# Performance work log

Hardware: AMD Instinct MI355X
Metric: run time of the kernel (lower is better)

Reference implementation:

```python
import jax, jax.numpy as jnp
import numpy as np

D_MODEL = 2048
N_Q_HEADS = 32
N_KV_HEADS = 8
D_HEAD = 64
D_MLP = 8192
NORM_EPS = 1e-5
INIT_RANGE = 0.02
IGNORE = -100000.0
B, S = 2, 2048


def setup_inputs() -> dict:
    key = jax.random.key(0)
    ks = jax.random.split(key, 8)
    return {
        "resid_pre": jax.random.normal(ks[0], (B, S, D_MODEL), dtype=jnp.float32),
        "W_Q": jax.random.normal(ks[1], (N_Q_HEADS, D_MODEL, D_HEAD), dtype=jnp.float32) * INIT_RANGE,
        "W_K": jax.random.normal(ks[2], (N_KV_HEADS, D_MODEL, D_HEAD), dtype=jnp.float32) * INIT_RANGE,
        "W_V": jax.random.normal(ks[3], (N_KV_HEADS, D_MODEL, D_HEAD), dtype=jnp.float32) * INIT_RANGE,
        "W_O": jax.random.normal(ks[4], (N_KV_HEADS, D_HEAD, D_MODEL), dtype=jnp.float32) * INIT_RANGE,
        "g1": jnp.ones((D_MODEL,), jnp.float32),
        "b1": jnp.zeros((D_MODEL,), jnp.float32),
        "g2": jnp.ones((D_MODEL,), jnp.float32),
        "b2": jnp.zeros((D_MODEL,), jnp.float32),
        "W_in": jax.random.normal(ks[5], (D_MODEL, D_MLP), dtype=jnp.float32) * INIT_RANGE,
        "b_in": jnp.zeros((D_MLP,), jnp.float32),
        "W_out": jax.random.normal(ks[6], (D_MLP, D_MODEL), dtype=jnp.float32) * INIT_RANGE,
        "b_out": jnp.zeros((D_MODEL,), jnp.float32),
    }


def rmsnorm(x, g, b):
    # torch.var (unbiased=False) is mean-centered variance, but x itself is
    # divided (not centered) -- faithful to the source.
    mu = jnp.mean(x, axis=-1, keepdims=True)
    var = jnp.mean(jnp.square(x - mu), axis=-1, keepdims=True)
    std = jnp.sqrt(var + NORM_EPS)
    return (x / std) * g + b


def attention(x, W_Q, W_K, W_V, W_O):
    b, s, _ = x.shape
    q = jnp.einsum('bpd,hde->bphe', x, W_Q)            # [b, s, n_q, d_head]
    k = jnp.einsum('bpd,hde->bphe', x, W_K)            # [b, s, n_kv, d_head]
    v = jnp.einsum('bpd,hde->bphe', x, W_V)            # [b, s, n_kv, d_head]
    g_size = N_Q_HEADS // N_KV_HEADS
    # rearrange '(n_kv g) d' with n_kv outer, group inner
    q = q.reshape(b, s, N_KV_HEADS, g_size, D_HEAD)
    # source einsum sums over the group dim (g not in output) -- faithful
    scores = jnp.einsum('bqkgd,bskd->bkqs', q, k) / jnp.sqrt(jnp.float32(D_HEAD))
    mask = jnp.triu(jnp.ones((s, s), dtype=bool), k=1)
    scores = jnp.where(mask, jnp.float32(IGNORE), scores)
    pattern = jax.nn.softmax(scores, axis=-1)          # [b, n_kv, q, s]
    z = jnp.einsum('bskd,bkqs->bqkd', v, pattern)      # [b, q, n_kv, d_head]
    return jnp.einsum('bqkd,kde->bqe', z, W_O)


def ffn(x, W_in, b_in, W_out, b_out):
    pre = jnp.einsum('bpd,dm->bpm', x, W_in) + b_in
    post = jax.nn.relu(pre)
    return jnp.einsum('bpm,md->bpd', post, W_out) + b_out


def reference(resid_pre, W_Q, W_K, W_V, W_O, g1, b1, g2, b2, W_in, b_in, W_out, b_out):
    resid_mid = attention(rmsnorm(resid_pre, g1, b1), W_Q, W_K, W_V, W_O) + resid_pre
    resid_post = ffn(rmsnorm(resid_mid, g2, b2), W_in, b_in, W_out, b_out) + resid_mid
    return resid_post
```

## Files before the change

### kernel.cpp

```cpp
#include <hip/hip_runtime.h>
#include <hip/hip_bf16.h>


using bf16 = __hip_bfloat16;
typedef __bf16 bf16x8_t __attribute__((ext_vector_type(8)));
typedef float  f32x4_t  __attribute__((ext_vector_type(4)));

#define D_MODEL 2048
#define SEQ     2048
#define NB      2
#define NTOK    4096
#define NKV     8
#define DHEAD   64
#define DMLP    8192
#define NQKV    1536

__device__ inline void storev(float* p, float v) { *p = v; }
__device__ inline void storev(bf16* p, float v)  { *p = __float2bfloat16(v); }

__device__ inline bf16 h_from_b(__bf16 x) {
    union { __bf16 b; bf16 h; } u;
    u.b = x;
    return u.h;
}

__global__ __launch_bounds__(256) void transpose_f32_bf16_kernel(
    const float* __restrict__ in, bf16* __restrict__ out, int K, int N)
{
    __shared__ float tile[32][33];
    const int n0 = blockIdx.x * 32, k0 = blockIdx.y * 32;
    const int tx = threadIdx.x & 31, ty = threadIdx.x >> 5;
    #pragma unroll
    for (int i = 0; i < 32; i += 8)
        tile[ty + i][tx] = in[(size_t)(k0 + ty + i) * N + n0 + tx];
    __syncthreads();
    #pragma unroll
    for (int i = 0; i < 32; i += 8)
        out[(size_t)(n0 + ty + i) * K + k0 + tx] = __float2bfloat16(tile[tx][ty + i]);
}

__global__ __launch_bounds__(256) void rmsnorm_kernel(
    const float* __restrict__ x, const float* __restrict__ g,
    const float* __restrict__ b, bf16* __restrict__ out)
{
    const int row = blockIdx.x;
    const int t = threadIdx.x;
    const float* xr = x + (size_t)row * D_MODEL;
    float4 a0 = *reinterpret_cast<const float4*>(xr + t * 8);
    float4 a1 = *reinterpret_cast<const float4*>(xr + t * 8 + 4);
    float v[8] = {a0.x, a0.y, a0.z, a0.w, a1.x, a1.y, a1.z, a1.w};
    float sum = 0.f, sumsq = 0.f;
    #pragma unroll
    for (int j = 0; j < 8; ++j) { sum += v[j]; sumsq += v[j] * v[j]; }
    #pragma unroll
    for (int o = 1; o < 64; o <<= 1) {
        sum   += __shfl_xor(sum, o);
        sumsq += __shfl_xor(sumsq, o);
    }
    __shared__ float rs[4], rq[4];
    if ((t & 63) == 0) { rs[t >> 6] = sum; rq[t >> 6] = sumsq; }
    __syncthreads();
    sum   = rs[0] + rs[1] + rs[2] + rs[3];
    sumsq = rq[0] + rq[1] + rq[2] + rq[3];
    const float mu  = sum * (1.f / D_MODEL);
    const float var = sumsq * (1.f / D_MODEL) - mu * mu;
    const float rstd = 1.f / sqrtf(var + 1e-5f);
    const int c = t * 8;
    float4 g0 = *reinterpret_cast<const float4*>(g + c);
    float4 g1 = *reinterpret_cast<const float4*>(g + c + 4);
    float4 b0 = *reinterpret_cast<const float4*>(b + c);
    float4 b1 = *reinterpret_cast<const float4*>(b + c + 4);
    float gg[8] = {g0.x, g0.y, g0.z, g0.w, g1.x, g1.y, g1.z, g1.w};
    float bb[8] = {b0.x, b0.y, b0.z, b0.w, b1.x, b1.y, b1.z, b1.w};
    bf16* op = out + (size_t)row * D_MODEL + c;
    #pragma unroll
    for (int j = 0; j < 8; ++j) op[j] = __float2bfloat16(v[j] * rstd * gg[j] + bb[j]);
}

__global__ __launch_bounds__(256) void fusedA_kernel(
    const float* __restrict__ resid_pre, const float* __restrict__ g1,
    const float* __restrict__ b1, bf16* __restrict__ x1,
    const float* __restrict__ WQ, const float* __restrict__ WK,
    const float* __restrict__ WV, bf16* __restrict__ wqkvT,
    const float* __restrict__ WO, bf16* __restrict__ woT)
{
    __shared__ __align__(16) float smem[32 * 65];
    const int id = blockIdx.x;
    const int t  = threadIdx.x;

    if (id < 4096) {
        float* rs = smem;
        float* rq = smem + 4;
        const float* xr = resid_pre + (size_t)id * D_MODEL;
        float4 a0 = *reinterpret_cast<const float4*>(xr + t * 8);
        float4 a1 = *reinterpret_cast<const float4*>(xr + t * 8 + 4);
        float v[8] = {a0.x, a0.y, a0.z, a0.w, a1.x, a1.y, a1.z, a1.w};
        float sum = 0.f, sumsq = 0.f;
        #pragma unroll
        for (int j = 0; j < 8; ++j) { sum += v[j]; sumsq += v[j] * v[j]; }
        #pragma unroll
        for (int o = 1; o < 64; o <<= 1) {
            sum   += __shfl_xor(sum, o);
            sumsq += __shfl_xor(sumsq, o);
        }
        if ((t & 63) == 0) { rs[t >> 6] = sum; rq[t >> 6] = sumsq; }
        __syncthreads();
        sum   = rs[0] + rs[1] + rs[2] + rs[3];
        sumsq = rq[0] + rq[1] + rq[2] + rq[3];
        const float mu  = sum * (1.f / D_MODEL);
        const float var = sumsq * (1.f / D_MODEL) - mu * mu;
        const float rstd = 1.f / sqrtf(var + 1e-5f);
        const int c = t * 8;
        float4 g0 = *reinterpret_cast<const float4*>(g1 + c);
        float4 g1v = *reinterpret_cast<const float4*>(g1 + c + 4);
        float4 b0 = *reinterpret_cast<const float4*>(b1 + c);
        float4 b1v = *reinterpret_cast<const float4*>(b1 + c + 4);
        float gg[8] = {g0.x, g0.y, g0.z, g0.w, g1v.x, g1v.y, g1v.z, g1v.w};
        float bb[8] = {b0.x, b0.y, b0.z, b0.w, b1v.x, b1v.y, b1v.z, b1v.w};
        bf16* op = x1 + (size_t)id * D_MODEL + c;
        #pragma unroll
        for (int j = 0; j < 8; ++j) op[j] = __float2bfloat16(v[j] * rstd * gg[j] + bb[j]);
    } else if (id < 5632) {
        int sub = id - 4096;
        const int which = sub >> 9;
        sub &= 511;
        const float* in = which == 0 ? WQ : (which == 1 ? WK : WV);
        bf16* outp = wqkvT + (size_t)which * 512 * D_MODEL;
        const int ngroup = which == 0 ? 4 : 1;
        const int kv = sub >> 6;
        const int k0 = (sub & 63) * 32;
        float (*tile)[65] = reinterpret_cast<float(*)[65]>(smem);
        const int e  = t & 63, kk = t >> 6;
        #pragma unroll
        for (int i = 0; i < 32; i += 4) {
            float s = 0.f;
            for (int g = 0; g < ngroup; ++g)
                s += in[((size_t)(kv * ngroup + g) * 2048 + k0 + kk + i) * 64 + e];
            tile[kk + i][e] = s;
        }
        __syncthreads();
        const int k = t & 31, ee = t >> 5;
        #pragma unroll
        for (int i = 0; i < 64; i += 8)
            outp[(size_t)(kv * 64 + ee + i) * 2048 + k0 + k] = __float2bfloat16(tile[k][ee + i]);
    } else {
        const int sub = id - 5632;
        const int n0 = (sub & 63) * 32, k0 = (sub >> 6) * 32;
        float (*tile)[33] = reinterpret_cast<float(*)[33]>(smem);
        const int tx = t & 31, ty = t >> 5;
        #pragma unroll
        for (int i = 0; i < 32; i += 8)
            tile[ty + i][tx] = WO[(size_t)(k0 + ty + i) * D_MODEL + n0 + tx];
        __syncthreads();
        #pragma unroll
        for (int i = 0; i < 32; i += 8)
            woT[(size_t)(n0 + ty + i) * 512 + k0 + tx] = __float2bfloat16(tile[tx][ty + i]);
    }
}

template<int BM, int BN, typename TC, bool BIAS, bool RELU, bool RESID>
__global__ __launch_bounds__(512, 2) void gemm_pipe_kernel(
    const bf16* __restrict__ A, const bf16* __restrict__ Bt,
    TC* __restrict__ C, const float* __restrict__ bias,
    const float* __restrict__ resid, int M, int N, int K, int nbx)
{
    constexpr int BK   = 64;
    constexpr int MREP = BM / 32;
    constexpr int NREP = BN / 64;
    constexpr int AI   = (BM * BK) / 4096;
    constexpr int BI   = (BN * BK) / 4096;
    constexpr int LD   = AI + BI;

    __shared__ __align__(16) bf16 As[2][BM * BK];
    __shared__ __align__(16) bf16 Bs[2][BN * BK];

    const int nwg = gridDim.x;
    const int swz = (blockIdx.x & 7) * (nwg >> 3) + (blockIdx.x >> 3);
    const int nby = nwg / nbx;
    const int by  = swz % nby;
    const int bx  = swz / nby;
    const int row0 = by * BM, col0 = bx * BN;

    const int t  = threadIdx.x;
    const int w  = t >> 6, ln = t & 63;
    const int wm = w >> 2, wn = w & 3;
    const int lr = ln & 15, hi = ln >> 4;

    const int srow = w * 8 + (ln >> 3);
    const int skx  = ((ln & 7) ^ (ln >> 3)) * 8;

    f32x4_t acc[MREP][NREP];
    #pragma unroll
    for (int m = 0; m < MREP; ++m)
        #pragma unroll
        for (int n = 0; n < NREP; ++n) acc[m][n] = (f32x4_t){0.f, 0.f, 0.f, 0.f};

    const int NT = K / BK;

    {
        const bf16* ga = A  + (size_t)(row0 + srow) * K + skx;
        const bf16* gb = Bt + (size_t)(col0 + srow) * K + skx;
        #pragma unroll
        for (int i = 0; i < AI; ++i)
            __builtin_amdgcn_global_load_lds(
                (const __attribute__((address_space(1))) void*)(ga + (size_t)i * 64 * K),
                (__attribute__((address_space(3))) void*)(&As[0][i * 4096 + w * 512]), 16, 0, 0);
        #pragma unroll
        for (int i = 0; i < BI; ++i)
            __builtin_amdgcn_global_load_lds(
                (const __attribute__((address_space(1))) void*)(gb + (size_t)i * 64 * K),
                (__attribute__((address_space(3))) void*)(&Bs[0][i * 4096 + w * 512]), 16, 0, 0);
    }

    for (int tt = 0; tt < NT; ++tt) {
        const int c = tt & 1;
        asm volatile("s_waitcnt lgkmcnt(0)" ::: "memory");
        __builtin_amdgcn_sched_barrier(0);
        __builtin_amdgcn_s_barrier();
        __builtin_amdgcn_sched_barrier(0);
        if (tt + 1 < NT) {
            const int d = c ^ 1;
            const int kt = (tt + 1) * BK;
            const bf16* ga = A  + (size_t)(row0 + srow) * K + kt + skx;
            const bf16* gb = Bt + (size_t)(col0 + srow) * K + kt + skx;
            #pragma unroll
            for (int i = 0; i < AI; ++i)
                __builtin_amdgcn_global_load_lds(
                    (const __attribute__((address_space(1))) void*)(ga + (size_t)i * 64 * K),
                    (__attribute__((address_space(3))) void*)(&As[d][i * 4096 + w * 512]), 16, 0, 0);
            #pragma unroll
            for (int i = 0; i < BI; ++i)
                __builtin_amdgcn_global_load_lds(
                    (const __attribute__((address_space(1))) void*)(gb + (size_t)i * 64 * K),
                    (__attribute__((address_space(3))) void*)(&Bs[d][i * 4096 + w * 512]), 16, 0, 0);
            __builtin_amdgcn_sched_barrier(0);
            if constexpr (LD == 8)      asm volatile("s_waitcnt vmcnt(8)" ::: "memory");
            else if constexpr (LD == 6) asm volatile("s_waitcnt vmcnt(6)" ::: "memory");
            else if constexpr (LD == 4) asm volatile("s_waitcnt vmcnt(4)" ::: "memory");
            else                        asm volatile("s_waitcnt vmcnt(3)" ::: "memory");
        } else {
            asm volatile("s_waitcnt vmcnt(0)" ::: "memory");
        }
        __builtin_amdgcn_sched_barrier(0);
        __builtin_amdgcn_s_barrier();
        __builtin_amdgcn_sched_barrier(0);

        #pragma unroll
        for (int kk = 0; kk < 2; ++kk) {
            bf16x8_t af[MREP], bfr[NREP];
            #pragma unroll
            for (int m = 0; m < MREP; ++m) {
                const int row = wm * (BM / 2) + m * 16 + lr;
                af[m] = *reinterpret_cast<const bf16x8_t*>(
                    &As[c][row * 64 + ((kk * 32 + hi * 8) ^ ((row & 7) << 3))]);
            }
            #pragma unroll
            for (int n = 0; n < NREP; ++n) {
                const int col = wn * (BN / 4) + n * 16 + lr;
                bfr[n] = *reinterpret_cast<const bf16x8_t*>(
                    &Bs[c][col * 64 + ((kk * 32 + hi * 8) ^ ((col & 7) << 3))]);
            }
            #pragma unroll
            for (int m = 0; m < MREP; ++m)
                #pragma unroll
                for (int n = 0; n < NREP; ++n)
                    acc[m][n] = __builtin_amdgcn_mfma_f32_16x16x32_bf16(af[m], bfr[n], acc[m][n], 0, 0, 0);
        }
    }

    #pragma unroll
    for (int m = 0; m < MREP; ++m) {
        #pragma unroll
        for (int n = 0; n < NREP; ++n) {
            const int cgl = col0 + wn * (BN / 4) + n * 16 + lr;
            #pragma unroll
            for (int j = 0; j < 4; ++j) {
                const int r = row0 + wm * (BM / 2) + m * 16 + hi * 4 + j;
                float v = acc[m][n][j];
                if constexpr (BIAS)  v += bias[cgl];
                if constexpr (RELU)  v = fmaxf(v, 0.f);
                if constexpr (RESID) v += resid[(size_t)r * N + cgl];
                storev(&C[(size_t)r * N + cgl], v);
            }
        }
    }
}

template<typename TC, bool BIAS, bool RELU, bool RESID>
__global__ __launch_bounds__(512, 2) void gemm_8ph_kernel(
    const bf16* __restrict__ A, const bf16* __restrict__ Bt,
    TC* __restrict__ C, const float* __restrict__ bias,
    const float* __restrict__ resid, int M, int N, int K, int nbx)
{
    __shared__ __align__(16) bf16 As[2][256 * 64];
    __shared__ __align__(16) bf16 Bs[2][256 * 64];

    const int nwg = gridDim.x;
    const int swz = (blockIdx.x & 7) * (nwg >> 3) + (blockIdx.x >> 3);
    const int nby = nwg / nbx;
    const int by  = swz % nby;
    const int bx  = swz / nby;
    const int row0 = by * 256, col0 = bx * 256;

    const int t  = threadIdx.x;
    const int w  = t >> 6, ln = t & 63;
    const int wm = w >> 2, wn = w & 3;
    const int lr = ln & 15, hi = ln >> 4;
    const int rx = (lr & 7) << 3;

    const int srow = w * 8 + (ln >> 3);
    const int skx  = ((ln & 7) ^ (ln >> 3)) * 8;

#define STAGE_A8(u, dbuf, kt)                                                   \
    __builtin_amdgcn_global_load_lds(                                           \
        (const __attribute__((address_space(1))) void*)(A + (size_t)(row0 + (u) * 64 + srow) * K + (kt) + skx), \
        (__attribute__((address_space(3))) void*)(&As[dbuf][(u) * 4096 + w * 512]), 16, 0, 0)
#define STAGE_B8(u, dbuf, kt)                                                   \
    __builtin_amdgcn_global_load_lds(                                           \
        (const __attribute__((address_space(1))) void*)(Bt + (size_t)(col0 + (u) * 64 + srow) * K + (kt) + skx), \
        (__attribute__((address_space(3))) void*)(&Bs[dbuf][(u) * 4096 + w * 512]), 16, 0, 0)
#define PH_BAR                                                                  \
    __builtin_amdgcn_sched_barrier(0);                                          \
    __builtin_amdgcn_s_barrier();                                               \
    __builtin_amdgcn_sched_barrier(0)
#define LGKM0                                                                   \
    asm volatile("s_waitcnt lgkmcnt(0)" ::: "memory");                          \
    __builtin_amdgcn_sched_barrier(0)

    f32x4_t acc[8][4];
    #pragma unroll
    for (int m = 0; m < 8; ++m)
        #pragma unroll
        for (int n = 0; n < 4; ++n) acc[m][n] = (f32x4_t){0.f, 0.f, 0.f, 0.f};

    bf16x8_t af[4][2];
    bf16x8_t af2[4][2];
    bf16x8_t bfr[4][2];

    const int NT = K / 64;

    STAGE_A8(0, 0, 0); STAGE_A8(2, 0, 0);
    STAGE_B8(0, 0, 0); STAGE_B8(1, 0, 0); STAGE_B8(2, 0, 0); STAGE_B8(3, 0, 0);
    STAGE_A8(1, 0, 0); STAGE_A8(3, 0, 0);
    asm volatile("s_waitcnt vmcnt(2)" ::: "memory");
    PH_BAR;

    for (int tt = 0; tt < NT; ++tt) {
        const int c  = tt & 1, d = c ^ 1;
        const int kn = (tt + 1) * 64;
        const bool pf = (tt + 1 < NT);

        #pragma unroll
        for (int mq = 0; mq < 4; ++mq) {
            const int row = wm * 128 + mq * 16 + lr;
            #pragma unroll
            for (int kk = 0; kk < 2; ++kk)
                af[mq][kk] = *reinterpret_cast<const bf16x8_t*>(
                    &As[c][row * 64 + ((kk * 32 + hi * 8) ^ rx)]);
        }
        #pragma unroll
        for (int n = 0; n < 2; ++n) {
            const int col = wn * 64 + n * 16 + lr;
            #pragma unroll
            for (int kk = 0; kk < 2; ++kk)
                bfr[n][kk] = *reinterpret_cast<const bf16x8_t*>(
                    &Bs[c][col * 64 + ((kk * 32 + hi * 8) ^ rx)]);
        }
        if (pf) { STAGE_A8(0, d, kn); STAGE_A8(2, d, kn); }
        PH_BAR;
        LGKM0;
        __builtin_amdgcn_s_setprio(1);
        #pragma unroll
        for (int mq = 0; mq < 4; ++mq)
            #pragma unroll
            for (int n = 0; n < 2; ++n)
                #pragma unroll
                for (int kk = 0; kk < 2; ++kk)
                    acc[mq][n] = __builtin_amdgcn_mfma_f32_16x16x32_bf16(af[mq][kk], bfr[n][kk], acc[mq][n], 0, 0, 0);
        __builtin_amdgcn_s_setprio(0);

        #pragma unroll
        for (int n = 2; n < 4; ++n) {
            const int col = wn * 64 + n * 16 + lr;
            #pragma unroll
            for (int kk = 0; kk < 2; ++kk)
                bfr[n][kk] = *reinterpret_cast<const bf16x8_t*>(
                    &Bs[c][col * 64 + ((kk * 32 + hi * 8) ^ rx)]);
        }
        if (pf) { STAGE_B8(0, d, kn); STAGE_B8(1, d, kn); }
        __builtin_amdgcn_sched_barrier(0);
        if (pf) { asm volatile("s_waitcnt vmcnt(4)" ::: "memory"); }
        else    { asm volatile("s_waitcnt vmcnt(0)" ::: "memory"); }
        PH_BAR;
        LGKM0;
        __builtin_amdgcn_s_setprio(1);
        #pragma unroll
        for (int mq = 0; mq < 4; ++mq)
            #pragma unroll
            for (int n = 2; n < 4; ++n)
                #pragma unroll
                for (int kk = 0; kk < 2; ++kk)
                    acc[mq][n] = __builtin_amdgcn_mfma_f32_16x16x32_bf16(af[mq][kk], bfr[n][kk], acc[mq][n], 0, 0, 0);
        __builtin_amdgcn_s_setprio(0);

        #pragma unroll
        for (int mq = 0; mq < 4; ++mq) {
            const int row = wm * 128 + 64 + mq * 16 + lr;
            #pragma unroll
            for (int kk = 0; kk < 2; ++kk)
                af2[mq][kk] = *reinterpret_cast<const bf16x8_t*>(
                    &As[c][row * 64 + ((kk * 32 + hi * 8) ^ rx)]);
        }
        if (pf) { STAGE_B8(2, d, kn); STAGE_B8(3, d, kn); }
        PH_BAR;
        LGKM0;
        __builtin_amdgcn_s_setprio(1);
        #pragma unroll
        for (int mq = 0; mq < 4; ++mq)
            #pragma unroll
            for (int n = 2; n < 4; ++n)
                #pragma unroll
                for (int kk = 0; kk < 2; ++kk)
                    acc[4 + mq][n] = __builtin_amdgcn_mfma_f32_16x16x32_bf16(af2[mq][kk], bfr[n][kk], acc[4 + mq][n], 0, 0, 0);
        __builtin_amdgcn_s_setprio(0);

        if (pf) {
            STAGE_A8(1, d, kn); STAGE_A8(3, d, kn);
            __builtin_amdgcn_sched_barrier(0);
            asm volatile("s_waitcnt vmcnt(2)" ::: "memory");
        }
        PH_BAR;
        __builtin_amdgcn_s_setprio(1);
        #pragma unroll
        for (int mq = 0; mq < 4; ++mq)
            #pragma unroll
            for (int n = 0; n < 2; ++n)
                #pragma unroll
                for (int kk = 0; kk < 2; ++kk)
                    acc[4 + mq][n] = __builtin_amdgcn_mfma_f32_16x16x32_bf16(af2[mq][kk], bfr[n][kk], acc[4 + mq][n], 0, 0, 0);
        __builtin_amdgcn_s_setprio(0);
    }

    #pragma unroll
    for (int m = 0; m < 8; ++m) {
        #pragma unroll
        for (int n = 0; n < 4; ++n) {
            const int cgl = col0 + wn * 64 + n * 16 + lr;
            #pragma unroll
            for (int j = 0; j < 4; ++j) {
                const int r = row0 + wm * 128 + m * 16 + hi * 4 + j;
                float v = acc[m][n][j];
                if constexpr (BIAS)  v += bias[cgl];
                if constexpr (RELU)  v = fmaxf(v, 0.f);
                if constexpr (RESID) v += resid[(size_t)r * N + cgl];
                storev(&C[(size_t)r * N + cgl], v);
            }
        }
    }
#undef STAGE_A8
#undef STAGE_B8
#undef PH_BAR
#undef LGKM0
}

#define KVBLK 64
#define LP    72

__global__ __launch_bounds__(256) void fusedB_kernel(
    const bf16* __restrict__ qkv, bf16* __restrict__ z,
    const float* __restrict__ W_in, bf16* __restrict__ winT)
{
    __shared__ __align__(16) char smem[3 * KVBLK * LP * 2];

    if (blockIdx.x >= 256) {
        const int sub = blockIdx.x - 256;
        const int n0 = (sub & 255) * 32, k0 = (sub >> 8) * 32;
        float (*tile)[33] = reinterpret_cast<float(*)[33]>(smem);
        const int tx = threadIdx.x & 31, ty = threadIdx.x >> 5;
        #pragma unroll
        for (int i = 0; i < 32; i += 8)
            tile[ty + i][tx] = W_in[(size_t)(k0 + ty + i) * DMLP + n0 + tx];
        __syncthreads();
        #pragma unroll
        for (int i = 0; i < 32; i += 8)
            winT[(size_t)(n0 + ty + i) * D_MODEL + k0 + tx] = __float2bfloat16(tile[tx][ty + i]);
        return;
    }

    const int i_   = blockIdx.x;
    const int pair = (i_ & 7) | ((i_ >> 7) << 3);
    const int a    = (i_ >> 3) & 15;
    const int kv   = pair & 7;
    const int b    = pair >> 3;
    const int b2   = 31 - a;
    const int t  = threadIdx.x;
    const int w  = t >> 6;
    const int ln = t & 63;
    const int lr = ln & 15;
    const int hi = ln >> 4;
    const int lk = hi * 8;

    bf16* Ks = reinterpret_cast<bf16*>(smem);
    bf16* Vt = Ks + KVBLK * LP;
    bf16* Ps = Vt + DHEAD * LP;

    bf16x8_t qfA[2], qfB[2];
    #pragma unroll
    for (int sb = 0; sb < 2; ++sb) {
        const int qrow = (sb ? b2 : a) * 64 + w * 16 + lr;
        const bf16* qp = qkv + (size_t)(b * SEQ + qrow) * NQKV + kv * 64;
        #pragma unroll
        for (int kk = 0; kk < 2; ++kk) {
            bf16x8_t v = *reinterpret_cast<const bf16x8_t*>(qp + kk * 32 + lk);
            if (sb) qfB[kk] = v; else qfA[kk] = v;
        }
    }

    f32x4_t accA[4], accB[4];
    #pragma unroll
    for (int n = 0; n < 4; ++n) {
        accA[n] = (f32x4_t){0.f, 0.f, 0.f, 0.f};
        accB[n] = (f32x4_t){0.f, 0.f, 0.f, 0.f};
    }
    float mA[4] = {-1e30f, -1e30f, -1e30f, -1e30f}, lA[4] = {0.f, 0.f, 0.f, 0.f};
    float mB[4] = {-1e30f, -1e30f, -1e30f, -1e30f}, lB[4] = {0.f, 0.f, 0.f, 0.f};

    const int qcdA = a  * 64 + w * 16 + hi * 4;
    const int qcdB = b2 * 64 + w * 16 + hi * 4;

    auto process = [&](const bf16x8_t* qf, f32x4_t* acc_o, float* m_st,
                       float* l_st, int qcd, int k0g, bool diag) {
        f32x4_t s[4];
        #pragma unroll
        for (int n = 0; n < 4; ++n) s[n] = (f32x4_t){0.f, 0.f, 0.f, 0.f};
        #pragma unroll
        for (int kk = 0; kk < 2; ++kk) {
            #pragma unroll
            for (int n = 0; n < 4; ++n) {
                bf16x8_t kf = *reinterpret_cast<const bf16x8_t*>(&Ks[(n * 16 + lr) * LP + kk * 32 + lk]);
                s[n] = __builtin_amdgcn_mfma_f32_16x16x32_bf16(qf[kk], kf, s[n], 0, 0, 0);
            }
        }
        #pragma unroll
        for (int n = 0; n < 4; ++n) {
            const int colg = k0g + n * 16 + lr;
            #pragma unroll
            for (int j = 0; j < 4; ++j) {
                float val = s[n][j] * 0.125f;
                if (diag && colg > qcd + j) val = -1e30f;
                s[n][j] = val;
            }
        }
        float alpha[4], mnew[4];
        #pragma unroll
        for (int j = 0; j < 4; ++j) {
            float mx = fmaxf(fmaxf(s[0][j], s[1][j]), fmaxf(s[2][j], s[3][j]));
            mx = fmaxf(mx, __shfl_xor(mx, 1));
            mx = fmaxf(mx, __shfl_xor(mx, 2));
            mx = fmaxf(mx, __shfl_xor(mx, 4));
            mx = fmaxf(mx, __shfl_xor(mx, 8));
            mnew[j]  = fmaxf(m_st[j], mx);
            alpha[j] = __expf(m_st[j] - mnew[j]);
            m_st[j]  = mnew[j];
        }
        float psum[4] = {0.f, 0.f, 0.f, 0.f};
        #pragma unroll
        for (int n = 0; n < 4; ++n) {
            #pragma unroll
            for (int j = 0; j < 4; ++j) {
                float p = __expf(s[n][j] - mnew[j]);
                psum[j] += p;
                Ps[(w * 16 + hi * 4 + j) * LP + n * 16 + lr] = __float2bfloat16(p);
            }
        }
        #pragma unroll
        for (int j = 0; j < 4; ++j) {
            float ps = psum[j];
            ps += __shfl_xor(ps, 1);
            ps += __shfl_xor(ps, 2);
            ps += __shfl_xor(ps, 4);
            ps += __shfl_xor(ps, 8);
            l_st[j] = l_st[j] * alpha[j] + ps;
        }
        #pragma unroll
        for (int n = 0; n < 4; ++n)
            #pragma unroll
            for (int j = 0; j < 4; ++j)
                acc_o[n][j] *= alpha[j];
        #pragma unroll
        for (int kk = 0; kk < 2; ++kk) {
            bf16x8_t pa = *reinterpret_cast<const bf16x8_t*>(&Ps[(w * 16 + lr) * LP + kk * 32 + lk]);
            #pragma unroll
            for (int n = 0; n < 4; ++n) {
                bf16x8_t vf = *reinterpret_cast<const bf16x8_t*>(&Vt[(n * 16 + lr) * LP + kk * 32 + lk]);
                acc_o[n] = __builtin_amdgcn_mfma_f32_16x16x32_bf16(pa, vf, acc_o[n], 0, 0, 0);
            }
        }
    };

    for (int kt = 0; kt <= b2; ++kt) {
        const int k0g = kt * KVBLK;
        __syncthreads();
        {
            const int r   = t >> 2;
            const int c16 = (t & 3) * 16;
            const bf16* kb = qkv + (size_t)(b * SEQ + k0g + r) * NQKV + 512 + kv * 64 + c16;
            *reinterpret_cast<bf16x8_t*>(&Ks[r * LP + c16])     = *reinterpret_cast<const bf16x8_t*>(kb);
            *reinterpret_cast<bf16x8_t*>(&Ks[r * LP + c16 + 8]) = *reinterpret_cast<const bf16x8_t*>(kb + 8);
        }
        {
            const int dv = w * 16;
            const bf16* vb = qkv + (size_t)(b * SEQ + k0g + ln) * NQKV + 1024 + kv * 64 + dv;
            bf16x8_t v0 = *reinterpret_cast<const bf16x8_t*>(vb);
            bf16x8_t v1 = *reinterpret_cast<const bf16x8_t*>(vb + 8);
            #pragma unroll
            for (int i = 0; i < 8; ++i) {
                Vt[(dv + i)     * LP + ln] = h_from_b(v0[i]);
                Vt[(dv + 8 + i) * LP + ln] = h_from_b(v1[i]);
            }
        }
        __syncthreads();

        if (kt <= a) process(qfA, accA, mA, lA, qcdA, k0g, kt == a);
        process(qfB, accB, mB, lB, qcdB, k0g, kt == b2);
    }

    #pragma unroll
    for (int j = 0; j < 4; ++j) {
        const float invA = 1.f / lA[j];
        bf16* zpA = z + (size_t)(b * SEQ + qcdA + j) * (NKV * DHEAD) + kv * 64;
        const float invB = 1.f / lB[j];
        bf16* zpB = z + (size_t)(b * SEQ + qcdB + j) * (NKV * DHEAD) + kv * 64;
        #pragma unroll
        for (int n = 0; n < 4; ++n) {
            zpA[n * 16 + lr] = __float2bfloat16(accA[n][j] * invA);
            zpB[n * 16 + lr] = __float2bfloat16(accB[n][j] * invB);
        }
    }
}

extern "C" void kernel_launch(void* const* d_in, const int* in_sizes, int n_in,
                              void* d_out, int out_size, void* d_ws, size_t ws_size,
                              hipStream_t stream)
{
    const float* resid_pre = (const float*)d_in[0];
    const float* W_Q   = (const float*)d_in[1];
    const float* W_K   = (const float*)d_in[2];
    const float* W_V   = (const float*)d_in[3];
    const float* W_O   = (const float*)d_in[4];
    const float* g1    = (const float*)d_in[5];
    const float* b1    = (const float*)d_in[6];
    const float* g2    = (const float*)d_in[7];
    const float* b2    = (const float*)d_in[8];
    const float* W_in  = (const float*)d_in[9];
    const float* b_in  = (const float*)d_in[10];
    const float* W_out = (const float*)d_in[11];
    const float* b_out = (const float*)d_in[12];
    float* out = (float*)d_out;

    char* ws = (char*)d_ws;
    const size_t OFF_WBIG  = 0;
    const size_t OFF_WOT   = OFF_WBIG + (size_t)DMLP * D_MODEL * 2;
    const size_t OFF_X1    = OFF_WOT  + (size_t)D_MODEL * 512 * 2;
    const size_t OFF_RMID  = OFF_X1   + (size_t)NTOK * D_MODEL * 2;
    const size_t OFF_POST  = OFF_RMID + (size_t)NTOK * D_MODEL * 4;
    const size_t OFF_WQKVT = OFF_POST;
    const size_t OFF_QKV   = OFF_WQKVT + (size_t)NQKV * D_MODEL * 2;
    const size_t OFF_Z     = OFF_QKV   + (size_t)NTOK * NQKV * 2;

    bf16*  winT   = (bf16*) (ws + OFF_WBIG);
    bf16*  woutT  = (bf16*) (ws + OFF_WBIG);
    bf16*  woT    = (bf16*) (ws + OFF_WOT);
    bf16*  x1     = (bf16*) (ws + OFF_X1);
    float* rmid   = (float*)(ws + OFF_RMID);
    bf16*  post   = (bf16*) (ws + OFF_POST);
    bf16*  wqkvT  = (bf16*) (ws + OFF_WQKVT);
    bf16*  qkv    = (bf16*) (ws + OFF_QKV);
    bf16*  zbuf   = (bf16*) (ws + OFF_Z);

    fusedA_kernel<<<4096 + 1536 + 1024, 256, 0, stream>>>(
        resid_pre, g1, b1, x1, W_Q, W_K, W_V, wqkvT, W_O, woT);
    gemm_pipe_kernel<128, 128, bf16, false, false, false><<<384, 512, 0, stream>>>(
        x1, wqkvT, qkv, nullptr, nullptr, NTOK, NQKV, D_MODEL, NQKV / 128);
    fusedB_kernel<<<256 + 16384, 256, 0, stream>>>(qkv, zbuf, W_in, winT);
    gemm_pipe_kernel<128, 128, float, false, false, true><<<512, 512, 0, stream>>>(
        zbuf, woT, rmid, nullptr, resid_pre, NTOK, D_MODEL, 512, D_MODEL / 128);
    rmsnorm_kernel<<<NTOK, 256, 0, stream>>>(rmid, g2, b2, x1);
    gemm_8ph_kernel<bf16, true, true, false><<<512, 512, 0, stream>>>(
        x1, winT, post, b_in, nullptr, NTOK, DMLP, D_MODEL, DMLP / 256);
    transpose_f32_bf16_kernel<<<dim3(D_MODEL / 32, DMLP / 32), 256, 0, stream>>>(W_out, woutT, DMLP, D_MODEL);
    gemm_pipe_kernel<128, 128, float, true, false, true><<<512, 512, 0, stream>>>(
        post, woutT, out, b_out, rmid, NTOK, D_MODEL, DMLP, D_MODEL / 128);
}
```

Baseline: 456.1 us.

## Fuse W_out transpose into FFN-in GEMM launch as extra tail blocks

Appends 4096 transpose blocks to the W_in GEMM grid so the W_out fp32-to-bf16 transpose runs in the same launch, filling idle CUs in the GEMM tail and removing a separate kernel launch. It uses a separate workspace region for the transposed W_out when the workspace is large enough, and falls back to the old path otherwise. The transpose blocks inherit the GEMM's large LDS and 512-thread footprint, which may limit how many co-reside.

Measured after the change: 460.5 us. Within noise of the previous version (+1.0%).

```diff
diff --git a/kernel.cpp b/kernel.cpp
--- a/kernel.cpp
+++ b/kernel.cpp
@@ -290,12 +290,29 @@
 __global__ __launch_bounds__(512, 2) void gemm_8ph_kernel(
     const bf16* __restrict__ A, const bf16* __restrict__ Bt,
     TC* __restrict__ C, const float* __restrict__ bias,
-    const float* __restrict__ resid, int M, int N, int K, int nbx)
+    const float* __restrict__ resid, int M, int N, int K, int nbx,
+    const float* __restrict__ Wt_src, bf16* __restrict__ Wt_dst, int ngemm)
 {
     __shared__ __align__(16) bf16 As[2][256 * 64];
     __shared__ __align__(16) bf16 Bs[2][256 * 64];
 
-    const int nwg = gridDim.x;
+    if ((int)blockIdx.x >= ngemm) {
+        const int sub = blockIdx.x - ngemm;
+        const int n0 = (sub & 31) * 64;
+        const int k0 = (sub >> 5) * 64;
+        float (*tile)[65] = reinterpret_cast<float(*)[65]>(&As[0][0]);
+        const int tx = threadIdx.x & 63, ty = threadIdx.x >> 6;
+        #pragma unroll
+        for (int i = 0; i < 64; i += 8)
+            tile[ty + i][tx] = Wt_src[(size_t)(k0 + ty + i) * D_MODEL + n0 + tx];
+        __syncthreads();
+        #pragma unroll
+        for (int i = 0; i < 64; i += 8)
+            Wt_dst[(size_t)(n0 + ty + i) * DMLP + k0 + tx] = __float2bfloat16(tile[tx][ty + i]);
+        return;
+    }
+
+    const int nwg = ngemm;
     const int swz = (blockIdx.x & 7) * (nwg >> 3) + (blockIdx.x >> 3);
     const int nby = nwg / nbx;
     const int by  = swz % nby;
@@ -667,9 +684,13 @@
     const size_t OFF_WQKVT = OFF_POST;
     const size_t OFF_QKV   = OFF_WQKVT + (size_t)NQKV * D_MODEL * 2;
     const size_t OFF_Z     = OFF_QKV   + (size_t)NTOK * NQKV * 2;
+    const size_t OFF_WOUTT = OFF_POST  + (size_t)NTOK * DMLP * 2;
+    const size_t NEED_PAR  = OFF_WOUTT + (size_t)D_MODEL * DMLP * 2;
+
+    const bool par = (ws_size >= NEED_PAR);
 
     bf16*  winT   = (bf16*) (ws + OFF_WBIG);
-    bf16*  woutT  = (bf16*) (ws + OFF_WBIG);
+    bf16*  woutT  = par ? (bf16*)(ws + OFF_WOUTT) : (bf16*)(ws + OFF_WBIG);
     bf16*  woT    = (bf16*) (ws + OFF_WOT);
     bf16*  x1     = (bf16*) (ws + OFF_X1);
     float* rmid   = (float*)(ws + OFF_RMID);
@@ -686,9 +707,11 @@
     gemm_pipe_kernel<128, 128, float, false, false, true><<<512, 512, 0, stream>>>(
         zbuf, woT, rmid, nullptr, resid_pre, NTOK, D_MODEL, 512, D_MODEL / 128);
     rmsnorm_kernel<<<NTOK, 256, 0, stream>>>(rmid, g2, b2, x1);
-    gemm_8ph_kernel<bf16, true, true, false><<<512, 512, 0, stream>>>(
-        x1, winT, post, b_in, nullptr, NTOK, DMLP, D_MODEL, DMLP / 256);
-    transpose_f32_bf16_kernel<<<dim3(D_MODEL / 32, DMLP / 32), 256, 0, stream>>>(W_out, woutT, DMLP, D_MODEL);
+    gemm_8ph_kernel<bf16, true, true, false><<<512 + (par ? 4096 : 0), 512, 0, stream>>>(
+        x1, winT, post, b_in, nullptr, NTOK, DMLP, D_MODEL, DMLP / 256,
+        W_out, woutT, 512);
+    if (!par)
+        transpose_f32_bf16_kernel<<<dim3(D_MODEL / 32, DMLP / 32), 256, 0, stream>>>(W_out, woutT, DMLP, D_MODEL);
     gemm_pipe_kernel<128, 128, float, true, false, true><<<512, 512, 0, stream>>>(
         post, woutT, out, b_out, rmid, NTOK, D_MODEL, DMLP, D_MODEL / 128);
 }
```
